# Optimization experiments

Hardware: AMD Instinct MI355X
Metric: run time of the kernel (lower is better)

Reference implementation:

```python
import jax, jax.numpy as jnp
import numpy as np

NUM_HEADS = 12
HEAD_DIM = 64
DIM = NUM_HEADS * HEAD_DIM  # 768
WIN = 14
REL = 2 * WIN - 1  # 27


def setup_inputs() -> dict:
    key = jax.random.key(0)
    ks = jax.random.split(key, 7)
    B, N = 256, WIN * WIN
    return {
        "x": jax.random.normal(ks[0], (B, N, DIM), dtype=jnp.float32),
        "qkv_w": jax.random.normal(ks[1], (3 * DIM, DIM), dtype=jnp.float32) * 0.02,
        "qkv_b": jnp.zeros((3 * DIM,), dtype=jnp.float32),
        "rel_pos_h": jax.random.normal(ks[2], (REL, HEAD_DIM), dtype=jnp.float32) * 0.02,
        "rel_pos_w": jax.random.normal(ks[3], (REL, HEAD_DIM), dtype=jnp.float32) * 0.02,
        "proj_w": jax.random.normal(ks[4], (DIM, DIM), dtype=jnp.float32) * 0.02,
        "proj_b": jnp.zeros((DIM,), dtype=jnp.float32),
        "H": WIN,
        "W": WIN,
    }


def _rel_pos_bias(q, rel_pos_h, rel_pos_w, H, W):
    # q: [B, heads, H*W, d] (already scaled). q_shape == k_shape == (H, W), ratios == 1.
    dist_h = jnp.arange(H)[:, None] - jnp.arange(H)[None, :] + (H - 1)  # [H, H]
    dist_w = jnp.arange(W)[:, None] - jnp.arange(W)[None, :] + (W - 1)  # [W, W]
    Rh = rel_pos_h[dist_h]  # [H, H, d]
    Rw = rel_pos_w[dist_w]  # [W, W, d]
    B, nh = q.shape[0], q.shape[1]
    r_q = q.reshape(B, nh, H, W, q.shape[-1])
    rel_h = jnp.einsum("bnhwd,hkd->bnhwk", r_q, Rh)  # [B, nh, H, W, Hk]
    rel_w = jnp.einsum("bnhwd,wkd->bnhwk", r_q, Rw)  # [B, nh, H, W, Wk]
    return rel_h[..., :, None] + rel_w[..., None, :]  # [B, nh, H, W, Hk, Wk]


def reference(x, qkv_w, qkv_b, rel_pos_h, rel_pos_w, proj_w, proj_b, H, W):
    B, N, C = x.shape
    d = C // NUM_HEADS
    scale = d ** -0.5
    qkv = x @ qkv_w.T + qkv_b  # [B, N, 3C]
    qkv = qkv.reshape(B, N, 3, NUM_HEADS, d).transpose(2, 0, 3, 1, 4)
    q, k, v = qkv[0], qkv[1], qkv[2]  # [B, nh, N, d]
    q = q * scale
    attn = jnp.einsum("bhqd,bhkd->bhqk", q, k)  # [B, nh, N, N]
    bias = _rel_pos_bias(q, rel_pos_h, rel_pos_w, H, W)
    attn = (attn.reshape(B, NUM_HEADS, H, W, H, W) + bias).reshape(B, NUM_HEADS, N, N)
    attn = jax.nn.softmax(attn, axis=-1)
    out = jnp.einsum("bhqk,bhkd->bhqd", attn, v)  # [B, nh, N, d]
    out = out.transpose(0, 2, 1, 3).reshape(B, N, C)
    return out @ proj_w.T + proj_b
```

## Files before the change

### kernel.cpp

```cpp
#include <hip/hip_runtime.h>
#include <stdint.h>


typedef __attribute__((ext_vector_type(8))) short bf16x8;
typedef __attribute__((ext_vector_type(4))) float f32x4;
typedef unsigned short u16;
typedef unsigned int u32;

__device__ __forceinline__ u16 f2bf(float f) {
  u32 x = __float_as_uint(f);
  x += 0x7fffu + ((x >> 16) & 1u);
  return (u16)(x >> 16);
}

__device__ __forceinline__ void gload_lds16(const void* g, void* l) {
  __builtin_amdgcn_global_load_lds(
      (__attribute__((address_space(1))) void*)g,
      (__attribute__((address_space(3))) void*)l, 16, 0, 0);
}

__global__ __launch_bounds__(256) void cvt_bf16(const float* __restrict__ src,
                                                u16* __restrict__ dst, int n4) {
  int i = blockIdx.x * 256 + threadIdx.x;
  if (i < n4) {
    float4 f = ((const float4*)src)[i];
    uint2 p;
    p.x = (u32)f2bf(f.x) | ((u32)f2bf(f.y) << 16);
    p.y = (u32)f2bf(f.z) | ((u32)f2bf(f.w) << 16);
    ((uint2*)dst)[i] = p;
  }
}

__device__ __forceinline__ void stage8(const u16* pA, const u16* pB,
                                       char* dstA, int k0) {
#pragma unroll
  for (int i = 0; i < 4; i++)
    gload_lds16(pA + (size_t)i * 49152 + k0, dstA + i * 8192);
#pragma unroll
  for (int i = 0; i < 4; i++)
    gload_lds16(pB + (size_t)i * 49152 + k0, dstA + 32768 + i * 8192);
}

template <int MODE, int NT>
__global__ __launch_bounds__(512, 2) void gemm256(
    const u16* __restrict__ A, const u16* __restrict__ W,
    const float* __restrict__ bias, u16* __restrict__ qb, u16* __restrict__ kb,
    u16* __restrict__ vb, float* __restrict__ outf) {
  __shared__ char lds[131072];

  const int t = threadIdx.x;
  const int lane = t & 63, wv = t >> 6;
  const int quad = lane >> 4, l15 = lane & 15;
  const int wm = wv >> 2, wn = wv & 3;

  const u32 nwg = gridDim.x;
  const u32 wg = blockIdx.x;
  const u32 qd = nwg >> 3, rm = nwg & 7;
  const u32 xcd = wg & 7, loc = wg >> 3;
  const u32 swz = (xcd < rm) ? (xcd * (qd + 1) + loc)
                             : (rm * (qd + 1) + (xcd - rm) * qd + loc);
  const int mtile = swz / NT;
  const int ntile = (int)swz - mtile * NT;
  const int m0 = mtile << 8, n0 = ntile << 8;

  const int srow = t >> 3;
  const int scol = ((t & 7) ^ (srow & 7)) << 3;
  const u16* pA = A + (size_t)(m0 + srow) * 768 + scol;
  const u16* pB = W + (size_t)(n0 + srow) * 768 + scol;
  char* sdst = lds + t * 16;

  const int swz0 = ((quad) ^ (l15 & 7)) << 4;
  const int swz1 = ((4 + quad) ^ (l15 & 7)) << 4;
  const int arow = (wm * 128 + l15) * 128;
  const int brow = 32768 + (wn * 64 + l15) * 128;

  f32x4 acc[8][4];
#pragma unroll
  for (int i = 0; i < 8; i++)
#pragma unroll
    for (int j = 0; j < 4; j++) acc[i][j] = (f32x4){0.f, 0.f, 0.f, 0.f};

  stage8(pA, pB, sdst, 0);
  asm volatile("s_waitcnt vmcnt(0)" ::: "memory");
  __builtin_amdgcn_s_barrier();

  bf16x8 af[4][2], bfr[4][2];
  for (int kt = 0; kt < 12; ++kt) {
    char* bufc = lds + ((kt & 1) << 16);
    char* nsdst = sdst + (((kt & 1) ^ 1) << 16);
    const int k0n = (kt + 1) << 6;

#pragma unroll
    for (int mf = 0; mf < 4; mf++) {
      af[mf][0] = *(const bf16x8*)(bufc + arow + mf * 2048 + swz0);
      af[mf][1] = *(const bf16x8*)(bufc + arow + mf * 2048 + swz1);
    }
#pragma unroll
    for (int nf = 0; nf < 2; nf++) {
      bfr[nf][0] = *(const bf16x8*)(bufc + brow + nf * 2048 + swz0);
      bfr[nf][1] = *(const bf16x8*)(bufc + brow + nf * 2048 + swz1);
    }
    if (kt < 11) stage8(pA, pB, nsdst, k0n);
    __builtin_amdgcn_s_barrier();
    asm volatile("s_waitcnt lgkmcnt(0)" ::: "memory");
    __builtin_amdgcn_s_setprio(1);
#pragma unroll
    for (int k = 0; k < 2; k++)
#pragma unroll
      for (int mf = 0; mf < 4; mf++)
#pragma unroll
        for (int nf = 0; nf < 2; nf++)
          acc[mf][nf] = __builtin_amdgcn_mfma_f32_16x16x32_bf16(
              af[mf][k], bfr[nf][k], acc[mf][nf], 0, 0, 0);
    __builtin_amdgcn_s_setprio(0);
    __builtin_amdgcn_s_barrier();

#pragma unroll
    for (int nf = 2; nf < 4; nf++) {
      bfr[nf][0] = *(const bf16x8*)(bufc + brow + nf * 2048 + swz0);
      bfr[nf][1] = *(const bf16x8*)(bufc + brow + nf * 2048 + swz1);
    }
    __builtin_amdgcn_s_barrier();
    asm volatile("s_waitcnt lgkmcnt(0)" ::: "memory");
    __builtin_amdgcn_s_setprio(1);
#pragma unroll
    for (int k = 0; k < 2; k++)
#pragma unroll
      for (int mf = 0; mf < 4; mf++)
#pragma unroll
        for (int nf = 2; nf < 4; nf++)
          acc[mf][nf] = __builtin_amdgcn_mfma_f32_16x16x32_bf16(
              af[mf][k], bfr[nf][k], acc[mf][nf], 0, 0, 0);
    __builtin_amdgcn_s_setprio(0);
    __builtin_amdgcn_s_barrier();

#pragma unroll
    for (int mf = 0; mf < 4; mf++) {
      af[mf][0] = *(const bf16x8*)(bufc + arow + (mf + 4) * 2048 + swz0);
      af[mf][1] = *(const bf16x8*)(bufc + arow + (mf + 4) * 2048 + swz1);
    }
    __builtin_amdgcn_s_barrier();
    asm volatile("s_waitcnt lgkmcnt(0)" ::: "memory");
    __builtin_amdgcn_s_setprio(1);
#pragma unroll
    for (int k = 0; k < 2; k++)
#pragma unroll
      for (int mf = 0; mf < 4; mf++)
#pragma unroll
        for (int nf = 0; nf < 2; nf++)
          acc[mf + 4][nf] = __builtin_amdgcn_mfma_f32_16x16x32_bf16(
              af[mf][k], bfr[nf][k], acc[mf + 4][nf], 0, 0, 0);
    __builtin_amdgcn_s_setprio(0);
    __builtin_amdgcn_s_barrier();

    __builtin_amdgcn_s_setprio(1);
#pragma unroll
    for (int k = 0; k < 2; k++)
#pragma unroll
      for (int mf = 0; mf < 4; mf++)
#pragma unroll
        for (int nf = 2; nf < 4; nf++)
          acc[mf + 4][nf] = __builtin_amdgcn_mfma_f32_16x16x32_bf16(
              af[mf][k], bfr[nf][k], acc[mf + 4][nf], 0, 0, 0);
    __builtin_amdgcn_s_setprio(0);
    asm volatile("s_waitcnt vmcnt(0)" ::: "memory");
    __builtin_amdgcn_s_barrier();
  }

  if (MODE == 0) {
    const int which = n0 / 768;
    u16* dst = (which == 0) ? qb : ((which == 1) ? kb : vb);
    const float sc = (which == 0) ? 0.125f : 1.0f;
    float bs[4];
    size_t hb[4];
#pragma unroll
    for (int nf = 0; nf < 4; nf++) {
      int n = n0 + wn * 64 + nf * 16 + l15;
      int cc = n - which * 768;
      bs[nf] = bias[n];
      hb[nf] = (size_t)(cc >> 6) * 12544 + (size_t)(cc & 63);
    }
#pragma unroll
    for (int mf = 0; mf < 8; mf++) {
#pragma unroll
      for (int r = 0; r < 4; r++) {
        int m = m0 + wm * 128 + mf * 16 + (quad << 2) + r;
        int bb = m / 196;
        int tok = m - bb * 196;
        size_t rb = (size_t)bb * 150528 + (size_t)tok * 64;
#pragma unroll
        for (int nf = 0; nf < 4; nf++)
          dst[rb + hb[nf]] = f2bf((acc[mf][nf][r] + bs[nf]) * sc);
      }
    }
  } else {
    float bs[4];
#pragma unroll
    for (int nf = 0; nf < 4; nf++)
      bs[nf] = bias[n0 + wn * 64 + nf * 16 + l15];
#pragma unroll
    for (int mf = 0; mf < 8; mf++) {
#pragma unroll
      for (int r = 0; r < 4; r++) {
        int m = m0 + wm * 128 + mf * 16 + (quad << 2) + r;
#pragma unroll
        for (int nf = 0; nf < 4; nf++)
          outf[(size_t)m * 768 + (n0 + wn * 64 + nf * 16 + l15)] =
              acc[mf][nf][r] + bs[nf];
      }
    }
  }
}

__global__ __launch_bounds__(256) void attn_fused(
    const u16* __restrict__ qbuf, const u16* __restrict__ kbuf,
    const u16* __restrict__ vbuf, const float* __restrict__ rel_h,
    const float* __restrict__ rel_w, u16* __restrict__ aout) {
  __shared__ u16 Vt[26 * 512];
  __shared__ u16 PsArr[4 * 26 * 128];

  const int t = threadIdx.x;
  const int bh = blockIdx.x;
  const int b = bh / 12, h = bh - b * 12;
  const int lane = t & 63, wv = t >> 6;
  const int quad = lane >> 4, l15 = lane & 15;
  const size_t base = (size_t)bh * (196 * 64);

  u16* Ps = PsArr + wv * (26 * 128);
  float* Tf = (float*)Ps;

  for (int c = t; c < 196 * 8; c += 256) {
    int row = c >> 3, seg = c & 7;
    uint4 vv = *(const uint4*)(vbuf + base + row * 64 + seg * 8);
    const u16* pv8 = (const u16*)&vv;
    u16* dst = Vt + (row >> 3) * 512 + (row & 7);
#pragma unroll
    for (int e = 0; e < 8; e++) dst[(seg * 8 + e) * 8] = pv8[e];
  }
  for (int i = t; i < 12 * 64; i += 256) {
    int k = 196 + (i >> 6), d = i & 63;
    Vt[(k >> 3) * 512 + d * 8 + (k & 7)] = 0;
  }

  bf16x8 brl[2][2][2];
#pragma unroll
  for (int half = 0; half < 2; half++) {
    const float* relp = half ? rel_w : rel_h;
#pragma unroll
    for (int nt = 0; nt < 2; nt++) {
      int ridx = nt * 16 + l15;
      if (ridx > 26) ridx = 26;
#pragma unroll
      for (int ks = 0; ks < 2; ks++) {
        const float* p = relp + ridx * 64 + ks * 32 + quad * 8;
        float4 f0 = *(const float4*)p;
        float4 f1 = *(const float4*)(p + 4);
        bf16x8 r;
        r[0] = (short)f2bf(f0.x); r[1] = (short)f2bf(f0.y);
        r[2] = (short)f2bf(f0.z); r[3] = (short)f2bf(f0.w);
        r[4] = (short)f2bf(f1.x); r[5] = (short)f2bf(f1.y);
        r[6] = (short)f2bf(f1.z); r[7] = (short)f2bf(f1.w);
        brl[half][nt][ks] = r;
      }
    }
  }
  __syncthreads();

  for (int qt = wv; qt < 13; qt += 4) {
    int qrl = qt * 16 + l15;
    if (qrl > 195) qrl = 195;
    bf16x8 aq0 = *(const bf16x8*)(qbuf + base + qrl * 64 + quad * 8);
    bf16x8 aq1 = *(const bf16x8*)(qbuf + base + qrl * 64 + 32 + quad * 8);

#pragma unroll
    for (int half = 0; half < 2; half++) {
#pragma unroll
      for (int nt = 0; nt < 2; nt++) {
        f32x4 tc = (f32x4){0.f, 0.f, 0.f, 0.f};
        tc = __builtin_amdgcn_mfma_f32_16x16x32_bf16(aq0, brl[half][nt][0], tc, 0, 0, 0);
        tc = __builtin_amdgcn_mfma_f32_16x16x32_bf16(aq1, brl[half][nt][1], tc, 0, 0, 0);
        int col = nt * 16 + l15;
        if (col < 27) {
#pragma unroll
          for (int r = 0; r < 4; r++)
            Tf[half * 448 + (quad * 4 + r) * 28 + col] = tc[r];
        }
      }
    }

    int trow[4], hqv[4], wqv[4];
#pragma unroll
    for (int r = 0; r < 4; r++) {
      int qr = qt * 16 + quad * 4 + r;
      if (qr > 195) qr = 195;
      hqv[r] = qr / 14;
      wqv[r] = qr - hqv[r] * 14;
      trow[r] = (quad * 4 + r) * 28;
    }

    u32 pw2[13][2];
    float sm[4] = {0.f, 0.f, 0.f, 0.f};
#pragma unroll
    for (int kt = 0; kt < 13; kt++) {
      int key = kt * 16 + l15;
      int keyc = (key > 195) ? 195 : key;
      bool valid = (key < 196);
      bf16x8 bk0 = *(const bf16x8*)(kbuf + base + keyc * 64 + quad * 8);
      bf16x8 bk1 = *(const bf16x8*)(kbuf + base + keyc * 64 + 32 + quad * 8);
      f32x4 s = (f32x4){0.f, 0.f, 0.f, 0.f};
      s = __builtin_amdgcn_mfma_f32_16x16x32_bf16(aq0, bk0, s, 0, 0, 0);
      s = __builtin_amdgcn_mfma_f32_16x16x32_bf16(aq1, bk1, s, 0, 0, 0);
      int hk = keyc / 14, wk = keyc - hk * 14;
      float pr[4];
#pragma unroll
      for (int r = 0; r < 4; r++) {
        float v = s[r] + Tf[trow[r] + (hqv[r] - hk + 13)] +
                  Tf[448 + trow[r] + (wqv[r] - wk + 13)];
        float p = valid ? __expf(v) : 0.f;
        pr[r] = p;
        sm[r] += p;
      }
      pw2[kt][0] = (u32)f2bf(pr[0]) | ((u32)f2bf(pr[1]) << 16);
      pw2[kt][1] = (u32)f2bf(pr[2]) | ((u32)f2bf(pr[3]) << 16);
    }

#pragma unroll
    for (int r = 0; r < 4; r++) {
      sm[r] += __shfl_xor(sm[r], 1, 64);
      sm[r] += __shfl_xor(sm[r], 2, 64);
      sm[r] += __shfl_xor(sm[r], 4, 64);
      sm[r] += __shfl_xor(sm[r], 8, 64);
    }
    float inv[4];
#pragma unroll
    for (int r = 0; r < 4; r++) inv[r] = 1.0f / sm[r];

#pragma unroll
    for (int kt = 0; kt < 13; kt++) {
      u16* pp = Ps + (kt * 2 + (l15 >> 3)) * 128 + (l15 & 7);
      pp[(quad * 4 + 0) * 8] = (u16)(pw2[kt][0] & 0xffff);
      pp[(quad * 4 + 1) * 8] = (u16)(pw2[kt][0] >> 16);
      pp[(quad * 4 + 2) * 8] = (u16)(pw2[kt][1] & 0xffff);
      pp[(quad * 4 + 3) * 8] = (u16)(pw2[kt][1] >> 16);
    }

    f32x4 oacc[4];
#pragma unroll
    for (int dt = 0; dt < 4; dt++) oacc[dt] = (f32x4){0.f, 0.f, 0.f, 0.f};
#pragma unroll
    for (int ks = 0; ks < 7; ks++) {
      bool mvalid = (ks < 6) || (quad < 2);
      bf16x8 ap = (bf16x8){0, 0, 0, 0, 0, 0, 0, 0};
      if (mvalid) ap = *(const bf16x8*)(Ps + (ks * 4 + quad) * 128 + l15 * 8);
#pragma unroll
      for (int dt = 0; dt < 4; dt++) {
        bf16x8 bv = (bf16x8){0, 0, 0, 0, 0, 0, 0, 0};
        if (mvalid)
          bv = *(const bf16x8*)(Vt + (ks * 4 + quad) * 512 + (dt * 16 + l15) * 8);
        oacc[dt] = __builtin_amdgcn_mfma_f32_16x16x32_bf16(ap, bv, oacc[dt], 0, 0, 0);
      }
    }

#pragma unroll
    for (int dt = 0; dt < 4; dt++) {
#pragma unroll
      for (int r = 0; r < 4; r++) {
        int qrow = qt * 16 + quad * 4 + r;
        if (qrow < 196) {
          float val = oacc[dt][r] * inv[r];
          aout[((size_t)(b * 196 + qrow) * 12 + h) * 64 + dt * 16 + l15] = f2bf(val);
        }
      }
    }
  }
}

extern "C" void kernel_launch(void* const* d_in, const int* in_sizes, int n_in,
                              void* d_out, int out_size, void* d_ws, size_t ws_size,
                              hipStream_t stream) {
  (void)in_sizes; (void)n_in; (void)out_size; (void)ws_size;
  const float* x      = (const float*)d_in[0];
  const float* qkv_w  = (const float*)d_in[1];
  const float* qkv_b  = (const float*)d_in[2];
  const float* rel_h  = (const float*)d_in[3];
  const float* rel_w  = (const float*)d_in[4];
  const float* proj_w = (const float*)d_in[5];
  const float* proj_b = (const float*)d_in[6];
  float* out = (float*)d_out;

  char* ws = (char*)d_ws;
  u16* xbf  = (u16*)(ws);
  u16* qbuf = (u16*)(ws + 77070336);
  u16* kbuf = (u16*)(ws + 154140672);
  u16* vbuf = (u16*)(ws + 231211008);
  u16* wqb  = (u16*)(ws + 308281344);
  u16* wpb  = (u16*)(ws + 311820288);

  cvt_bf16<<<37632, 256, 0, stream>>>(x, xbf, 38535168 / 4);
  cvt_bf16<<<1728, 256, 0, stream>>>(qkv_w, wqb, 1769472 / 4);
  cvt_bf16<<<576, 256, 0, stream>>>(proj_w, wpb, 589824 / 4);

  gemm256<0, 9><<<1764, 512, 0, stream>>>(xbf, wqb, qkv_b, qbuf, kbuf, vbuf,
                                          nullptr);
  attn_fused<<<3072, 256, 0, stream>>>(qbuf, kbuf, vbuf, rel_h, rel_w, xbf);
  gemm256<1, 3><<<588, 512, 0, stream>>>(xbf, wpb, proj_b, nullptr, nullptr,
                                         nullptr, out);
}
```

Before: 840.3 us.

## Transpose attention MFMAs to keep P in registers via shuffles

Result: slower. 1.707 ms (+103.2%).

```diff
diff --git a/kernel.cpp b/kernel.cpp
--- a/kernel.cpp
+++ b/kernel.cpp
@@ -4,6 +4,7 @@
 
 typedef __attribute__((ext_vector_type(8))) short bf16x8;
 typedef __attribute__((ext_vector_type(4))) float f32x4;
+typedef __attribute__((ext_vector_type(4))) unsigned int u32x4;
 typedef unsigned short u16;
 typedef unsigned int u32;
 
@@ -11,6 +12,10 @@
   u32 x = __float_as_uint(f);
   x += 0x7fffu + ((x >> 16) & 1u);
   return (u16)(x >> 16);
+}
+
+__device__ __forceinline__ u32 pack2bf(float a, float b) {
+  return (u32)f2bf(a) | ((u32)f2bf(b) << 16);
 }
 
 __device__ __forceinline__ void gload_lds16(const void* g, void* l) {
@@ -25,8 +30,8 @@
   if (i < n4) {
     float4 f = ((const float4*)src)[i];
     uint2 p;
-    p.x = (u32)f2bf(f.x) | ((u32)f2bf(f.y) << 16);
-    p.y = (u32)f2bf(f.z) | ((u32)f2bf(f.w) << 16);
+    p.x = pack2bf(f.x, f.y);
+    p.y = pack2bf(f.z, f.w);
     ((uint2*)dst)[i] = p;
   }
 }
@@ -212,12 +217,12 @@
   }
 }
 
-__global__ __launch_bounds__(256) void attn_fused(
+__global__ __launch_bounds__(256, 3) void attn_fused(
     const u16* __restrict__ qbuf, const u16* __restrict__ kbuf,
     const u16* __restrict__ vbuf, const float* __restrict__ rel_h,
     const float* __restrict__ rel_w, u16* __restrict__ aout) {
   __shared__ u16 Vt[26 * 512];
-  __shared__ u16 PsArr[4 * 26 * 128];
+  __shared__ float TL[4][2][28][16];
 
   const int t = threadIdx.x;
   const int bh = blockIdx.x;
@@ -225,9 +230,6 @@
   const int lane = t & 63, wv = t >> 6;
   const int quad = lane >> 4, l15 = lane & 15;
   const size_t base = (size_t)bh * (196 * 64);
-
-  u16* Ps = PsArr + wv * (26 * 128);
-  float* Tf = (float*)Ps;
 
   for (int c = t; c < 196 * 8; c += 256) {
     int row = c >> 3, seg = c & 7;
@@ -266,110 +268,108 @@
   }
   __syncthreads();
 
+  float (*TLh)[16] = TL[wv][0];
+  float (*TLw)[16] = TL[wv][1];
+  const u16* kB = kbuf + base;
+  const u16* qB = qbuf + base;
+
   for (int qt = wv; qt < 13; qt += 4) {
     int qrl = qt * 16 + l15;
     if (qrl > 195) qrl = 195;
-    bf16x8 aq0 = *(const bf16x8*)(qbuf + base + qrl * 64 + quad * 8);
-    bf16x8 aq1 = *(const bf16x8*)(qbuf + base + qrl * 64 + 32 + quad * 8);
+    bf16x8 aq0 = *(const bf16x8*)(qB + qrl * 64 + quad * 8);
+    bf16x8 aq1 = *(const bf16x8*)(qB + qrl * 64 + 32 + quad * 8);
+    const int hq = qrl / 14, wq = qrl - hq * 14;
 
 #pragma unroll
     for (int half = 0; half < 2; half++) {
 #pragma unroll
       for (int nt = 0; nt < 2; nt++) {
         f32x4 tc = (f32x4){0.f, 0.f, 0.f, 0.f};
-        tc = __builtin_amdgcn_mfma_f32_16x16x32_bf16(aq0, brl[half][nt][0], tc, 0, 0, 0);
-        tc = __builtin_amdgcn_mfma_f32_16x16x32_bf16(aq1, brl[half][nt][1], tc, 0, 0, 0);
-        int col = nt * 16 + l15;
-        if (col < 27) {
-#pragma unroll
-          for (int r = 0; r < 4; r++)
-            Tf[half * 448 + (quad * 4 + r) * 28 + col] = tc[r];
+        tc = __builtin_amdgcn_mfma_f32_16x16x32_bf16(brl[half][nt][0], aq0, tc, 0, 0, 0);
+        tc = __builtin_amdgcn_mfma_f32_16x16x32_bf16(brl[half][nt][1], aq1, tc, 0, 0, 0);
+#pragma unroll
+        for (int r = 0; r < 4; r++) {
+          int r27 = nt * 16 + quad * 4 + r;
+          if (r27 < 27) TL[wv][half][r27][l15] = tc[r];
         }
       }
     }
 
-    int trow[4], hqv[4], wqv[4];
-#pragma unroll
-    for (int r = 0; r < 4; r++) {
-      int qr = qt * 16 + quad * 4 + r;
-      if (qr > 195) qr = 195;
-      hqv[r] = qr / 14;
-      wqv[r] = qr - hqv[r] * 14;
-      trow[r] = (quad * 4 + r) * 28;
-    }
-
     u32 pw2[13][2];
-    float sm[4] = {0.f, 0.f, 0.f, 0.f};
+    float sm = 0.f;
 #pragma unroll
     for (int kt = 0; kt < 13; kt++) {
-      int key = kt * 16 + l15;
-      int keyc = (key > 195) ? 195 : key;
-      bool valid = (key < 196);
-      bf16x8 bk0 = *(const bf16x8*)(kbuf + base + keyc * 64 + quad * 8);
-      bf16x8 bk1 = *(const bf16x8*)(kbuf + base + keyc * 64 + 32 + quad * 8);
+      int keyl = kt * 16 + l15;
+      int keyc = (keyl > 195) ? 195 : keyl;
+      bf16x8 bk0 = *(const bf16x8*)(kB + keyc * 64 + quad * 8);
+      bf16x8 bk1 = *(const bf16x8*)(kB + keyc * 64 + 32 + quad * 8);
       f32x4 s = (f32x4){0.f, 0.f, 0.f, 0.f};
-      s = __builtin_amdgcn_mfma_f32_16x16x32_bf16(aq0, bk0, s, 0, 0, 0);
-      s = __builtin_amdgcn_mfma_f32_16x16x32_bf16(aq1, bk1, s, 0, 0, 0);
-      int hk = keyc / 14, wk = keyc - hk * 14;
+      s = __builtin_amdgcn_mfma_f32_16x16x32_bf16(bk0, aq0, s, 0, 0, 0);
+      s = __builtin_amdgcn_mfma_f32_16x16x32_bf16(bk1, aq1, s, 0, 0, 0);
+      const int key0 = kt * 16 + quad * 4;
+      const int hk0 = key0 / 14, wk0 = key0 - 14 * hk0;
+      const bool valid = (kt < 12) || (quad == 0);
       float pr[4];
 #pragma unroll
       for (int r = 0; r < 4; r++) {
-        float v = s[r] + Tf[trow[r] + (hqv[r] - hk + 13)] +
-                  Tf[448 + trow[r] + (wqv[r] - wk + 13)];
+        int cr = (wk0 + r >= 14) ? 1 : 0;
+        int hk = hk0 + cr, wk = wk0 + r - 14 * cr;
+        float v = s[r] + TLh[hq - hk + 13][l15] + TLw[wq - wk + 13][l15];
         float p = valid ? __expf(v) : 0.f;
         pr[r] = p;
-        sm[r] += p;
-      }
-      pw2[kt][0] = (u32)f2bf(pr[0]) | ((u32)f2bf(pr[1]) << 16);
-      pw2[kt][1] = (u32)f2bf(pr[2]) | ((u32)f2bf(pr[3]) << 16);
-    }
-
-#pragma unroll
-    for (int r = 0; r < 4; r++) {
-      sm[r] += __shfl_xor(sm[r], 1, 64);
-      sm[r] += __shfl_xor(sm[r], 2, 64);
-      sm[r] += __shfl_xor(sm[r], 4, 64);
-      sm[r] += __shfl_xor(sm[r], 8, 64);
-    }
-    float inv[4];
-#pragma unroll
-    for (int r = 0; r < 4; r++) inv[r] = 1.0f / sm[r];
-
-#pragma unroll
-    for (int kt = 0; kt < 13; kt++) {
-      u16* pp = Ps + (kt * 2 + (l15 >> 3)) * 128 + (l15 & 7);
-      pp[(quad * 4 + 0) * 8] = (u16)(pw2[kt][0] & 0xffff);
-      pp[(quad * 4 + 1) * 8] = (u16)(pw2[kt][0] >> 16);
-      pp[(quad * 4 + 2) * 8] = (u16)(pw2[kt][1] & 0xffff);
-      pp[(quad * 4 + 3) * 8] = (u16)(pw2[kt][1] >> 16);
-    }
+        sm += p;
+      }
+      pw2[kt][0] = pack2bf(pr[0], pr[1]);
+      pw2[kt][1] = pack2bf(pr[2], pr[3]);
+    }
+    sm += __shfl_xor(sm, 16, 64);
+    sm += __shfl_xor(sm, 32, 64);
+    const float inv = 1.0f / sm;
 
     f32x4 oacc[4];
 #pragma unroll
     for (int dt = 0; dt < 4; dt++) oacc[dt] = (f32x4){0.f, 0.f, 0.f, 0.f};
-#pragma unroll
-    for (int ks = 0; ks < 7; ks++) {
-      bool mvalid = (ks < 6) || (quad < 2);
-      bf16x8 ap = (bf16x8){0, 0, 0, 0, 0, 0, 0, 0};
-      if (mvalid) ap = *(const bf16x8*)(Ps + (ks * 4 + quad) * 128 + l15 * 8);
+    const int srcA = l15 + ((quad & 1) << 5);
+    const bool hi = (quad >> 1) != 0;
+#pragma unroll
+    for (int st = 0; st < 7; st++) {
+      u32 w0, w1, w2, w3;
+      if (st < 6) {
+        u32 a0 = __shfl(pw2[2 * st][0], srcA), b0 = __shfl(pw2[2 * st + 1][0], srcA);
+        u32 a1 = __shfl(pw2[2 * st][1], srcA), b1 = __shfl(pw2[2 * st + 1][1], srcA);
+        u32 a2 = __shfl(pw2[2 * st][0], srcA + 16), b2 = __shfl(pw2[2 * st + 1][0], srcA + 16);
+        u32 a3 = __shfl(pw2[2 * st][1], srcA + 16), b3 = __shfl(pw2[2 * st + 1][1], srcA + 16);
+        w0 = hi ? b0 : a0; w1 = hi ? b1 : a1;
+        w2 = hi ? b2 : a2; w3 = hi ? b3 : a3;
+      } else {
+        u32 a0 = __shfl(pw2[12][0], srcA);
+        u32 a1 = __shfl(pw2[12][1], srcA);
+        u32 a2 = __shfl(pw2[12][0], srcA + 16);
+        u32 a3 = __shfl(pw2[12][1], srcA + 16);
+        w0 = hi ? 0u : a0; w1 = hi ? 0u : a1;
+        w2 = hi ? 0u : a2; w3 = hi ? 0u : a3;
+      }
+      u32x4 pbw = (u32x4){w0, w1, w2, w3};
+      bf16x8 pb = __builtin_bit_cast(bf16x8, pbw);
+      const bool mvalid = (st < 6) || (quad < 2);
 #pragma unroll
       for (int dt = 0; dt < 4; dt++) {
-        bf16x8 bv = (bf16x8){0, 0, 0, 0, 0, 0, 0, 0};
+        bf16x8 av = (bf16x8){0, 0, 0, 0, 0, 0, 0, 0};
         if (mvalid)
-          bv = *(const bf16x8*)(Vt + (ks * 4 + quad) * 512 + (dt * 16 + l15) * 8);
-        oacc[dt] = __builtin_amdgcn_mfma_f32_16x16x32_bf16(ap, bv, oacc[dt], 0, 0, 0);
-      }
-    }
-
-#pragma unroll
-    for (int dt = 0; dt < 4; dt++) {
-#pragma unroll
-      for (int r = 0; r < 4; r++) {
-        int qrow = qt * 16 + quad * 4 + r;
-        if (qrow < 196) {
-          float val = oacc[dt][r] * inv[r];
-          aout[((size_t)(b * 196 + qrow) * 12 + h) * 64 + dt * 16 + l15] = f2bf(val);
-        }
+          av = *(const bf16x8*)(Vt + (st * 4 + quad) * 512 + (dt * 16 + l15) * 8);
+        oacc[dt] = __builtin_amdgcn_mfma_f32_16x16x32_bf16(av, pb, oacc[dt], 0, 0, 0);
+      }
+    }
+
+    const int qrow = qt * 16 + l15;
+    if (qrow < 196) {
+      u16* op = aout + ((size_t)(b * 196 + qrow) * 12 + h) * 64;
+#pragma unroll
+      for (int dt = 0; dt < 4; dt++) {
+        uint2 stv;
+        stv.x = pack2bf(oacc[dt][0] * inv, oacc[dt][1] * inv);
+        stv.y = pack2bf(oacc[dt][2] * inv, oacc[dt][3] * inv);
+        *(uint2*)(op + dt * 16 + quad * 4) = stv;
       }
     }
   }
```
